# Performance work log

Hardware: AMD Instinct MI355X
Metric: run time of the kernel (lower is better)

Reference implementation:

```python
import jax, jax.numpy as jnp
import numpy as np

B, L, D_MODEL, H = 2, 2048, 1024, 16
HD = D_MODEL // H  # head dim = 64


def setup_inputs() -> dict:
    key = jax.random.key(0)
    ks = jax.random.split(key, 11)
    s = 1.0 / np.sqrt(D_MODEL)
    inp = {
        "Q": jax.random.normal(ks[0], (B, L, D_MODEL), jnp.float32),
        "K": jax.random.normal(ks[1], (B, L, D_MODEL), jnp.float32),
        "V": jax.random.normal(ks[2], (B, L, D_MODEL), jnp.float32),
        "Wq": jax.random.normal(ks[3], (D_MODEL, D_MODEL), jnp.float32) * s,
        "bq": jnp.zeros((D_MODEL,), jnp.float32),
        "Wk": jax.random.normal(ks[4], (D_MODEL, D_MODEL), jnp.float32) * s,
        "bk": jnp.zeros((D_MODEL,), jnp.float32),
        "Wv": jax.random.normal(ks[5], (D_MODEL, D_MODEL), jnp.float32) * s,
        "bv": jnp.zeros((D_MODEL,), jnp.float32),
        "Wo": jax.random.normal(ks[6], (D_MODEL, D_MODEL), jnp.float32) * s,
        "bo": jnp.zeros((D_MODEL,), jnp.float32),
    }
    return inp


def _split_heads(x):
    # [B, L, H*D] -> [B, H, L, D]
    return x.reshape(B, L, H, HD).transpose(0, 2, 1, 3)


def reference(Q, K, V, Wq, bq, Wk, bk, Wv, bv, Wo, bo):
    q = _split_heads(Q @ Wq.T + bq)
    k = _split_heads(K @ Wk.T + bk)
    v = _split_heads(V @ Wv.T + bv)
    scale = 1.0 / jnp.sqrt(jnp.asarray(HD, q.dtype))
    # full [B, H, L, L] score matrix, as in the original bmm->softmax->bmm
    scores = jnp.einsum("bhqd,bhkd->bhqk", q, k) * scale
    attn = jax.nn.softmax(scores, axis=-1)
    o = jnp.einsum("bhqk,bhkd->bhqd", attn, v)
    o = o.transpose(0, 2, 1, 3).reshape(B, L, D_MODEL)  # concat heads
    return o @ Wo.T + bo
```

## Files before the change

kernel.cpp:

```cpp
#include <hip/hip_runtime.h>
#include <math.h>
#include <stdint.h>

typedef __bf16 bf16_t;
typedef __attribute__((ext_vector_type(2))) __bf16 bf16x2;
typedef __attribute__((ext_vector_type(8))) __bf16 bf16x8;
typedef __attribute__((ext_vector_type(4))) float f32x4;
typedef __attribute__((ext_vector_type(16))) float f32x16;
typedef __attribute__((address_space(1))) unsigned int gu32;
typedef __attribute__((address_space(3))) unsigned int lu32;

#define MFMA16(a, b, c) __builtin_amdgcn_mfma_f32_16x16x32_bf16((a), (b), (c), 0, 0, 0)
#define MFMA32(a, b, c) __builtin_amdgcn_mfma_f32_32x32x16_bf16((a), (b), (c), 0, 0, 0)

__device__ __forceinline__ void gll16(const void* g, void* l) {
    __builtin_amdgcn_global_load_lds((const gu32*)(uintptr_t)g,
                                     (lu32*)(uintptr_t)l, 16, 0, 0);
}

__device__ __forceinline__ bf16x8 ld_frag68(const bf16_t* p) {
    union { bf16x8 v; uint2 u[2]; } r;
    r.u[0] = *(const uint2*)p;
    r.u[1] = *(const uint2*)(p + 4);
    return r.v;
}

__global__ __launch_bounds__(256) void convert_all(
    const float* __restrict__ Q, const float* __restrict__ K, const float* __restrict__ V,
    const float* __restrict__ Wq, const float* __restrict__ Wk, const float* __restrict__ Wv,
    const float* __restrict__ Wo, bf16_t* __restrict__ dst) {
    size_t e0 = (size_t)blockIdx.x * 2048;
    const float* src; size_t off;
    if (e0 < 4194304)       { src = Q;  off = e0; }
    else if (e0 < 8388608)  { src = K;  off = e0 - 4194304; }
    else if (e0 < 12582912) { src = V;  off = e0 - 8388608; }
    else if (e0 < 13631488) { src = Wq; off = e0 - 12582912; }
    else if (e0 < 14680064) { src = Wk; off = e0 - 13631488; }
    else if (e0 < 15728640) { src = Wv; off = e0 - 14680064; }
    else                    { src = Wo; off = e0 - 15728640; }
#pragma unroll
    for (int p = 0; p < 2; ++p) {
        int t = p * 1024 + threadIdx.x * 4;
        float4 v = *(const float4*)(src + off + t);
        union { ushort4 u; bf16_t h[4]; } pk;
        pk.h[0] = (bf16_t)v.x; pk.h[1] = (bf16_t)v.y;
        pk.h[2] = (bf16_t)v.z; pk.h[3] = (bf16_t)v.w;
        *(ushort4*)(dst + e0 + t) = pk.u;
    }
}

__global__ __launch_bounds__(256) void qkv_gemm(
    const bf16_t* __restrict__ Qb, const bf16_t* __restrict__ Kb, const bf16_t* __restrict__ Vb,
    const bf16_t* __restrict__ Wqb, const bf16_t* __restrict__ Wkb, const bf16_t* __restrict__ Wvb,
    const float* __restrict__ bq, const float* __restrict__ bk, const float* __restrict__ bv,
    bf16_t* __restrict__ qo, bf16_t* __restrict__ ko, bf16_t* __restrict__ vT) {
    constexpr int Kdim = 1024, N = 1024;
    __shared__ __attribute__((aligned(16))) bf16_t smem[4 * 128 * 64];

    const int tid = threadIdx.x, wave = tid >> 6, lane = tid & 63;
    const int z = blockIdx.z;
    const bf16_t* A = (z == 0) ? Qb : (z == 1) ? Kb : Vb;
    const bf16_t* W = (z == 0) ? Wqb : (z == 1) ? Wkb : Wvb;
    const float* bias = (z == 0) ? bq : (z == 1) ? bk : bv;
    const int bm = blockIdx.x * 128, bn = blockIdx.y * 128;
    const int l16 = lane & 15, quad = lane >> 4;
    const int wm = (wave >> 1) * 64, wn = (wave & 1) * 64;
    const int grow = lane >> 3;
    const int gcol = (((lane & 7) ^ grow)) * 8;
    const int rsw = l16 & 7;

    f32x4 acc[4][4] = {};

    auto stage = [&](int k0, bf16_t* As, bf16_t* Bs) {
#pragma unroll
        for (int j = 0; j < 4; ++j) {
            int chunk = wave * 4 + j;
            int row = chunk * 8 + grow;
            gll16(A + (size_t)(bm + row) * Kdim + k0 + gcol, As + chunk * 512);
            gll16(W + (size_t)(bn + row) * Kdim + k0 + gcol, Bs + chunk * 512);
        }
    };
    auto compute = [&](const bf16_t* As, const bf16_t* Bs) {
#pragma unroll
        for (int ks = 0; ks < 64; ks += 32) {
            const int so = (((ks >> 3) + quad) ^ rsw) * 8;
            bf16x8 af[4], bf[4];
#pragma unroll
            for (int i = 0; i < 4; ++i)
                af[i] = *(const bf16x8*)&As[(wm + i * 16 + l16) * 64 + so];
#pragma unroll
            for (int i = 0; i < 4; ++i)
                bf[i] = *(const bf16x8*)&Bs[(wn + i * 16 + l16) * 64 + so];
#pragma unroll
            for (int i = 0; i < 4; ++i)
#pragma unroll
                for (int j = 0; j < 4; ++j)
                    acc[i][j] = MFMA16(af[i], bf[j], acc[i][j]);
        }
    };

    stage(0, smem, smem + 8192);
    asm volatile("s_waitcnt vmcnt(0)" ::: "memory");
    __builtin_amdgcn_s_barrier();
    int cur = 0;
    for (int t = 0; t < 15; ++t) {
        bf16_t* nb = smem + (cur ^ 1) * 16384;
        stage((t + 1) * 64, nb, nb + 8192);
        bf16_t* cb = smem + cur * 16384;
        compute(cb, cb + 8192);
        asm volatile("s_waitcnt vmcnt(0)" ::: "memory");
        __builtin_amdgcn_s_barrier();
        cur ^= 1;
    }
    {
        bf16_t* cb = smem + cur * 16384;
        compute(cb, cb + 8192);
    }

    if (z < 2) {
        bf16_t* outp = (z == 0) ? qo : ko;
        const float sc = (z == 0) ? 0.18033688011112042f : 1.0f;
        constexpr int RST = 132;
#pragma unroll
        for (int p = 0; p < 2; ++p) {
            __syncthreads();
            if ((wave >> 1) == p) {
#pragma unroll
                for (int mi = 0; mi < 4; ++mi)
#pragma unroll
                    for (int nj = 0; nj < 4; ++nj) {
                        int col = wn + nj * 16 + l16;
                        float bv_ = bias[bn + col];
#pragma unroll
                        for (int r = 0; r < 4; ++r) {
                            int rp = mi * 16 + quad * 4 + r;
                            smem[rp * RST + col] = (bf16_t)((acc[mi][nj][r] + bv_) * sc);
                        }
                    }
            }
            __syncthreads();
            int rp = tid >> 2;
            int cb2 = (tid & 3) * 32;
            int row = bm + p * 64 + rp;
#pragma unroll
            for (int j = 0; j < 4; ++j) {
                uint2 lo = *(const uint2*)&smem[rp * RST + cb2 + j * 8];
                uint2 hi = *(const uint2*)&smem[rp * RST + cb2 + j * 8 + 4];
                *(uint4*)&outp[(size_t)row * N + bn + cb2 + j * 8] =
                    make_uint4(lo.x, lo.y, hi.x, hi.y);
            }
        }
    } else {
#pragma unroll
        for (int mi = 0; mi < 4; ++mi)
#pragma unroll
            for (int nj = 0; nj < 4; ++nj) {
                int col = bn + wn + nj * 16 + l16;
                int h = col >> 6, d = col & 63;
                float bv_ = bias[col];
                int row0 = bm + wm + mi * 16 + quad * 4;
                int bb = row0 >> 11, l = row0 & 2047;
                int lb = (l & ~12) | ((l & 4) << 1) | ((l & 8) >> 1);
                union { ushort4 u; bf16_t h4[4]; } pk;
#pragma unroll
                for (int r = 0; r < 4; ++r) pk.h4[r] = (bf16_t)(acc[mi][nj][r] + bv_);
                *(ushort4*)&vT[(((size_t)bb * 16 + h) * 64 + d) * 2048 + lb] = pk.u;
            }
    }
}

__global__ __launch_bounds__(256) void out_gemm(const bf16_t* __restrict__ Op,
                                                const float* __restrict__ lpp,
                                                const bf16_t* __restrict__ W,
                                                const float* __restrict__ bias,
                                                float* __restrict__ out) {
    constexpr int Kdim = 1024, N = 1024;
    __shared__ __attribute__((aligned(16))) bf16_t smem[2 * 12288];
    const int tid = threadIdx.x, wave = tid >> 6, lane = tid & 63;
    const int bm = blockIdx.x * 64, bn = blockIdx.y * 128;
    const int l16 = lane & 15, quad = lane >> 4;
    const int wm = (wave >> 1) * 32, wn = (wave & 1) * 64;
    const int grow = lane >> 3;
    const int gcol = (((lane & 7) ^ grow)) * 8;
    const int rsw = l16 & 7;
    f32x4 acc[2][4] = {};

    const int arow0 = bm + (wave * 2 + 0) * 8 + grow;
    const int arow1 = bm + (wave * 2 + 1) * 8 + grow;

    uint4 a0p, a0q, a1p, a1q;
    float ivn0, ivn1;

    auto loadA = [&](int k0) {
        const int h = k0 >> 6;
        a0p = *(const uint4*)(Op + (size_t)arow0 * Kdim + k0 + gcol);
        a0q = *(const uint4*)(Op + 4194304 + (size_t)arow0 * Kdim + k0 + gcol);
        a1p = *(const uint4*)(Op + (size_t)arow1 * Kdim + k0 + gcol);
        a1q = *(const uint4*)(Op + 4194304 + (size_t)arow1 * Kdim + k0 + gcol);
        const int li0 = ((arow0 >> 11) * 16 + h) * 2048 + (arow0 & 2047);
        const int li1 = ((arow1 >> 11) * 16 + h) * 2048 + (arow1 & 2047);
        ivn0 = 1.f / (lpp[li0] + lpp[65536 + li0]);
        ivn1 = 1.f / (lpp[li1] + lpp[65536 + li1]);
    };
    auto writeA = [&](bf16_t* As) {
        union { uint4 u; bf16_t h8[8]; } x, y, w0, w1;
        x.u = a0p; y.u = a0q;
#pragma unroll
        for (int i = 0; i < 8; ++i)
            w0.h8[i] = (bf16_t)(((float)x.h8[i] + (float)y.h8[i]) * ivn0);
        x.u = a1p; y.u = a1q;
#pragma unroll
        for (int i = 0; i < 8; ++i)
            w1.h8[i] = (bf16_t)(((float)x.h8[i] + (float)y.h8[i]) * ivn1);
        *(uint4*)&As[(wave * 2 + 0) * 512 + lane * 8] = w0.u;
        *(uint4*)&As[(wave * 2 + 1) * 512 + lane * 8] = w1.u;
    };
    auto stageW = [&](int k0, bf16_t* Bs) {
#pragma unroll
        for (int j = 0; j < 4; ++j) {
            int chunk = wave * 4 + j;
            int row = chunk * 8 + grow;
            gll16(W + (size_t)(bn + row) * Kdim + k0 + gcol, Bs + chunk * 512);
        }
    };
    auto compute = [&](const bf16_t* As, const bf16_t* Bs) {
#pragma unroll
        for (int ks = 0; ks < 64; ks += 32) {
            const int so0 = (((ks >> 3) + quad) ^ rsw) * 8;
            bf16x8 af[2], bf[4];
#pragma unroll
            for (int i = 0; i < 2; ++i)
                af[i] = *(const bf16x8*)&As[(wm + i * 16 + l16) * 64 + so0];
#pragma unroll
            for (int i = 0; i < 4; ++i)
                bf[i] = *(const bf16x8*)&Bs[(wn + i * 16 + l16) * 64 + so0];
#pragma unroll
            for (int i = 0; i < 2; ++i)
#pragma unroll
                for (int j = 0; j < 4; ++j)
                    acc[i][j] = MFMA16(af[i], bf[j], acc[i][j]);
        }
    };

    loadA(0);
    stageW(0, smem + 4096);
    writeA(smem);
    __syncthreads();
    int cur = 0;
    for (int t = 0; t < 15; ++t) {
        bf16_t* nb = smem + (cur ^ 1) * 12288;
        loadA((t + 1) * 64);
        stageW((t + 1) * 64, nb + 4096);
        bf16_t* cb = smem + cur * 12288;
        compute(cb, cb + 4096);
        writeA(nb);
        asm volatile("s_waitcnt vmcnt(0)" ::: "memory");
        __syncthreads();
        cur ^= 1;
    }
    {
        bf16_t* cb = smem + cur * 12288;
        compute(cb, cb + 4096);
    }

#pragma unroll
    for (int mi = 0; mi < 2; ++mi)
#pragma unroll
        for (int nj = 0; nj < 4; ++nj) {
            int col = bn + wn + nj * 16 + l16;
            float bv_ = bias[col];
#pragma unroll
            for (int r = 0; r < 4; ++r) {
                int row = bm + wm + mi * 16 + quad * 4 + r;
                out[(size_t)row * N + col] = acc[mi][nj][r] + bv_;
            }
        }
}

__global__ __launch_bounds__(256, 2) void attn8(const bf16_t* __restrict__ qo,
                                                const bf16_t* __restrict__ ko,
                                                const bf16_t* __restrict__ vT,
                                                bf16_t* __restrict__ Op,
                                                float* __restrict__ lpp) {
    constexpr int L = 2048, D = 1024, ST = 68;
    constexpr int BUF = 2 * 64 * ST;
    __shared__ __attribute__((aligned(16))) bf16_t smem[2 * BUF];

    const int tid = threadIdx.x, wave = tid >> 6, lane = tid & 63;
    const int l31 = lane & 31, hi = lane >> 5;
    const int b = blockIdx.x >> 4, h = blockIdx.x & 15;
    const int q0 = blockIdx.y * 256;
    const int split = blockIdx.z;
    bf16_t* Opart = Op + (size_t)split * 4194304;
    float* lpart = lpp + split * 65536;

    const int rloc = tid >> 2, cg = tid & 3;
    const bf16_t* kbase = ko + ((size_t)b * L + rloc) * D + h * 64 + cg * 16;
    const bf16_t* vbase = vT + (((size_t)b * 16 + h) * 64 + rloc) * L + cg * 16;

    bf16x8 qfa[4], qfb[4];
    {
        const bf16_t* qa = qo + ((size_t)b * L + q0 + wave * 32 + l31) * D + h * 64 + hi * 8;
        const bf16_t* qb2 = qa + (size_t)128 * D;
#pragma unroll
        for (int ks = 0; ks < 4; ++ks) {
            qfa[ks] = *(const bf16x8*)(qa + ks * 16);
            qfb[ks] = *(const bf16x8*)(qb2 + ks * 16);
        }
    }

    f32x16 o0a{}, o1a{}, o0b{}, o1b{};
    float lpla = 0.f, lplb = 0.f;

    const int kt0 = split * 16, kt1 = kt0 + 16;

    uint4 ka, kc, va, vc;
    auto gload = [&](int kt) {
        const size_t koff = (size_t)(kt * 64) * D;
        const int voff = kt * 64;
        ka = *(const uint4*)(kbase + koff);
        kc = *(const uint4*)(kbase + koff + 8);
        va = *(const uint4*)(vbase + voff);
        vc = *(const uint4*)(vbase + voff + 8);
    };
    auto swrite = [&](bf16_t* buf) {
        bf16_t* kd = &buf[rloc * ST + cg * 16];
        bf16_t* vd = &buf[64 * ST + rloc * ST + cg * 16];
        *(uint2*)(kd + 0)  = make_uint2(ka.x, ka.y);
        *(uint2*)(kd + 4)  = make_uint2(ka.z, ka.w);
        *(uint2*)(kd + 8)  = make_uint2(kc.x, kc.y);
        *(uint2*)(kd + 12) = make_uint2(kc.z, kc.w);
        *(uint2*)(vd + 0)  = make_uint2(va.x, va.y);
        *(uint2*)(vd + 4)  = make_uint2(va.z, va.w);
        *(uint2*)(vd + 8)  = make_uint2(vc.x, vc.y);
        *(uint2*)(vd + 12) = make_uint2(vc.z, vc.w);
    };

    gload(kt0);
    swrite(smem);
    gload(kt0 + 1 < kt1 ? kt0 + 1 : kt1 - 1);
    asm volatile("s_waitcnt lgkmcnt(0)" ::: "memory");
    __builtin_amdgcn_s_barrier();

    int cur = 0;
    for (int kt = kt0; kt < kt1; ++kt) {
        swrite(smem + (cur ^ 1) * BUF);
        gload(kt + 2 < kt1 ? kt + 2 : kt1 - 1);
        const bf16_t* ksm = smem + cur * BUF;
        const bf16_t* vsm = ksm + 64 * ST;

        f32x16 s0a{}, s1a{}, s0b{}, s1b{};
        __builtin_amdgcn_s_setprio(1);
#pragma unroll
        for (int ks = 0; ks < 4; ++ks) {
            bf16x8 k0 = ld_frag68(&ksm[l31 * ST + ks * 16 + hi * 8]);
            bf16x8 k1 = ld_frag68(&ksm[(32 + l31) * ST + ks * 16 + hi * 8]);
            s0a = MFMA32(k0, qfa[ks], s0a);
            s1a = MFMA32(k1, qfa[ks], s1a);
            s0b = MFMA32(k0, qfb[ks], s0b);
            s1b = MFMA32(k1, qfb[ks], s1b);
        }
        __builtin_amdgcn_s_setprio(0);

#pragma unroll
        for (int t = 0; t < 4; ++t) {
            union { bf16x8 v; bf16_t e[8]; } pfa, pfb;
#pragma unroll
            for (int j = 0; j < 8; ++j) {
                float sva = (t < 2) ? s0a[(t & 1) * 8 + j] : s1a[(t & 1) * 8 + j];
                float svb = (t < 2) ? s0b[(t & 1) * 8 + j] : s1b[(t & 1) * 8 + j];
                float pa = __builtin_amdgcn_exp2f(sva);
                float pb = __builtin_amdgcn_exp2f(svb);
                lpla += pa; lplb += pb;
                pfa.e[j] = (bf16_t)pa;
                pfb.e[j] = (bf16_t)pb;
            }
            bf16x8 v0 = ld_frag68(&vsm[l31 * ST + t * 16 + hi * 8]);
            bf16x8 v1 = ld_frag68(&vsm[(32 + l31) * ST + t * 16 + hi * 8]);
            __builtin_amdgcn_s_setprio(1);
            o0a = MFMA32(v0, pfa.v, o0a);
            o1a = MFMA32(v1, pfa.v, o1a);
            o0b = MFMA32(v0, pfb.v, o0b);
            o1b = MFMA32(v1, pfb.v, o1b);
            __builtin_amdgcn_s_setprio(0);
        }

        asm volatile("s_waitcnt lgkmcnt(0)" ::: "memory");
        __builtin_amdgcn_s_barrier();
        cur ^= 1;
    }

    lpla += __shfl_xor(lpla, 32, 64);
    lplb += __shfl_xor(lplb, 32, 64);
    if (hi == 0) {
        lpart[((size_t)b * 16 + h) * 2048 + q0 + wave * 32 + l31] = lpla;
        lpart[((size_t)b * 16 + h) * 2048 + q0 + 128 + wave * 32 + l31] = lplb;
    }

    __syncthreads();
    bf16_t* ew = smem + wave * (32 * ST);
#pragma unroll
    for (int r = 0; r < 16; r += 2) {
        int d = (r & 3) + 8 * (r >> 2) + 4 * hi;
        *(bf16x2*)&ew[l31 * ST + d] = bf16x2{(bf16_t)o0a[r], (bf16_t)o0a[r + 1]};
        *(bf16x2*)&ew[l31 * ST + 32 + d] = bf16x2{(bf16_t)o1a[r], (bf16_t)o1a[r + 1]};
    }
#pragma unroll
    for (int p = 0; p < 4; ++p) {
        int rr = p * 8 + (lane >> 3);
        int cc = (lane & 7) * 8;
        uint2 lo = *(const uint2*)&ew[rr * ST + cc];
        uint2 hi2 = *(const uint2*)&ew[rr * ST + cc + 4];
        *(uint4*)&Opart[((size_t)b * L + q0 + wave * 32 + rr) * D + h * 64 + cc] =
            make_uint4(lo.x, lo.y, hi2.x, hi2.y);
    }
#pragma unroll
    for (int r = 0; r < 16; r += 2) {
        int d = (r & 3) + 8 * (r >> 2) + 4 * hi;
        *(bf16x2*)&ew[l31 * ST + d] = bf16x2{(bf16_t)o0b[r], (bf16_t)o0b[r + 1]};
        *(bf16x2*)&ew[l31 * ST + 32 + d] = bf16x2{(bf16_t)o1b[r], (bf16_t)o1b[r + 1]};
    }
#pragma unroll
    for (int p = 0; p < 4; ++p) {
        int rr = p * 8 + (lane >> 3);
        int cc = (lane & 7) * 8;
        uint2 lo = *(const uint2*)&ew[rr * ST + cc];
        uint2 hi2 = *(const uint2*)&ew[rr * ST + cc + 4];
        *(uint4*)&Opart[((size_t)b * L + q0 + 128 + wave * 32 + rr) * D + h * 64 + cc] =
            make_uint4(lo.x, lo.y, hi2.x, hi2.y);
    }
}

extern "C" void kernel_launch(void* const* d_in, const int* in_sizes, int n_in,
                              void* d_out, int out_size, void* d_ws, size_t ws_size,
                              hipStream_t stream) {
    const float* Q  = (const float*)d_in[0];
    const float* Kx = (const float*)d_in[1];
    const float* V  = (const float*)d_in[2];
    const float* Wq = (const float*)d_in[3];
    const float* bq = (const float*)d_in[4];
    const float* Wk = (const float*)d_in[5];
    const float* bk = (const float*)d_in[6];
    const float* Wv = (const float*)d_in[7];
    const float* bv = (const float*)d_in[8];
    const float* Wo = (const float*)d_in[9];
    const float* bo = (const float*)d_in[10];

    bf16_t* ws0 = (bf16_t*)d_ws;
    bf16_t* Qb  = ws0;
    bf16_t* Kb  = ws0 + 4194304;
    bf16_t* Vb  = ws0 + 8388608;
    bf16_t* Wqb = ws0 + 12582912;
    bf16_t* Wkb = ws0 + 13631488;
    bf16_t* Wvb = ws0 + 14680064;
    bf16_t* Wob = ws0 + 15728640;
    bf16_t* vT  = ws0 + 16777216;
    bf16_t* Op  = Qb;
    float*  lpp = (float*)Wqb;
    bf16_t* qo = (bf16_t*)d_out;
    bf16_t* ko = qo + 4194304;

    convert_all<<<8192, 256, 0, stream>>>(Q, Kx, V, Wq, Wk, Wv, Wo, ws0);
    qkv_gemm<<<dim3(32, 8, 3), 256, 0, stream>>>(Qb, Kb, Vb, Wqb, Wkb, Wvb,
                                                 bq, bk, bv, qo, ko, vT);
    attn8<<<dim3(32, 8, 2), 256, 0, stream>>>(qo, ko, vT, Op, lpp);
    out_gemm<<<dim3(64, 8), 256, 0, stream>>>(Op, lpp, Wob, bo, (float*)d_out);
}
```

Baseline: 221.1 us.

## Enlarge QKV GEMM tiles to 256x256 with 8 waves and interleaved prefetch

The QKV projection GEMM moves from 128x128 tiles with 4 waves to 256x256 tiles with 8 waves. Each wave now computes a 128x64 sub-tile. The main loop is restructured so the A and B prefetch loads are split and interleaved between MFMA groups, and s_setprio is raised around the MFMA bursts. The aim is more reuse per loaded byte and better overlap of loads with compute. The cost is 128KB of LDS, higher register pressure from the doubled accumulators, and only 192 blocks, which may not fill all CUs.

```diff
diff --git a/kernel.cpp b/kernel.cpp
--- a/kernel.cpp
+++ b/kernel.cpp
@@ -49,84 +49,137 @@
     }
 }
 
-__global__ __launch_bounds__(256) void qkv_gemm(
+__global__ __launch_bounds__(512, 2) void qkv_gemm(
     const bf16_t* __restrict__ Qb, const bf16_t* __restrict__ Kb, const bf16_t* __restrict__ Vb,
     const bf16_t* __restrict__ Wqb, const bf16_t* __restrict__ Wkb, const bf16_t* __restrict__ Wvb,
     const float* __restrict__ bq, const float* __restrict__ bk, const float* __restrict__ bv,
     bf16_t* __restrict__ qo, bf16_t* __restrict__ ko, bf16_t* __restrict__ vT) {
     constexpr int Kdim = 1024, N = 1024;
-    __shared__ __attribute__((aligned(16))) bf16_t smem[4 * 128 * 64];
+    __shared__ __attribute__((aligned(16))) bf16_t smem[2 * 32768];
 
     const int tid = threadIdx.x, wave = tid >> 6, lane = tid & 63;
     const int z = blockIdx.z;
     const bf16_t* A = (z == 0) ? Qb : (z == 1) ? Kb : Vb;
     const bf16_t* W = (z == 0) ? Wqb : (z == 1) ? Wkb : Wvb;
     const float* bias = (z == 0) ? bq : (z == 1) ? bk : bv;
-    const int bm = blockIdx.x * 128, bn = blockIdx.y * 128;
+    const int bm = blockIdx.x * 256, bn = blockIdx.y * 256;
     const int l16 = lane & 15, quad = lane >> 4;
-    const int wm = (wave >> 1) * 64, wn = (wave & 1) * 64;
+    const int wr = wave >> 2, wc = wave & 3;
+    const int wm = wr * 128, wn = wc * 64;
     const int grow = lane >> 3;
     const int gcol = (((lane & 7) ^ grow)) * 8;
     const int rsw = l16 & 7;
 
-    f32x4 acc[4][4] = {};
-
-    auto stage = [&](int k0, bf16_t* As, bf16_t* Bs) {
+    f32x4 acc[8][4] = {};
+
+    auto stageA = [&](int k0, bf16_t* As) {
 #pragma unroll
         for (int j = 0; j < 4; ++j) {
             int chunk = wave * 4 + j;
             int row = chunk * 8 + grow;
             gll16(A + (size_t)(bm + row) * Kdim + k0 + gcol, As + chunk * 512);
+        }
+    };
+    auto stageB = [&](int k0, bf16_t* Bs) {
+#pragma unroll
+        for (int j = 0; j < 4; ++j) {
+            int chunk = wave * 4 + j;
+            int row = chunk * 8 + grow;
             gll16(W + (size_t)(bn + row) * Kdim + k0 + gcol, Bs + chunk * 512);
         }
     };
-    auto compute = [&](const bf16_t* As, const bf16_t* Bs) {
-#pragma unroll
-        for (int ks = 0; ks < 64; ks += 32) {
-            const int so = (((ks >> 3) + quad) ^ rsw) * 8;
-            bf16x8 af[4], bf[4];
-#pragma unroll
-            for (int i = 0; i < 4; ++i)
-                af[i] = *(const bf16x8*)&As[(wm + i * 16 + l16) * 64 + so];
-#pragma unroll
-            for (int i = 0; i < 4; ++i)
-                bf[i] = *(const bf16x8*)&Bs[(wn + i * 16 + l16) * 64 + so];
+
+    stageA(0, smem);
+    stageB(0, smem + 16384);
+    asm volatile("s_waitcnt vmcnt(0)" ::: "memory");
+    __builtin_amdgcn_s_barrier();
+
+    int cur = 0;
+    for (int t = 0; t < 16; ++t) {
+        const bf16_t* cA = smem + cur * 32768;
+        const bf16_t* cB = cA + 16384;
+        bf16_t* nA = smem + (cur ^ 1) * 32768;
+        bf16_t* nB = nA + 16384;
+        const int k1 = (t + 1) * 64;
+        const bool pf = (t < 15);
+
+        bf16x8 af[4], bf[4];
+        if (pf) stageA(k1, nA);
+        {
+            const int so = ((0 + quad) ^ rsw) * 8;
+#pragma unroll
+            for (int i = 0; i < 4; ++i)
+                bf[i] = *(const bf16x8*)&cB[(wn + i * 16 + l16) * 64 + so];
+#pragma unroll
+            for (int i = 0; i < 4; ++i)
+                af[i] = *(const bf16x8*)&cA[(wm + i * 16 + l16) * 64 + so];
+            __builtin_amdgcn_s_setprio(1);
 #pragma unroll
             for (int i = 0; i < 4; ++i)
 #pragma unroll
                 for (int j = 0; j < 4; ++j)
                     acc[i][j] = MFMA16(af[i], bf[j], acc[i][j]);
-        }
-    };
-
-    stage(0, smem, smem + 8192);
-    asm volatile("s_waitcnt vmcnt(0)" ::: "memory");
-    __builtin_amdgcn_s_barrier();
-    int cur = 0;
-    for (int t = 0; t < 15; ++t) {
-        bf16_t* nb = smem + (cur ^ 1) * 16384;
-        stage((t + 1) * 64, nb, nb + 8192);
-        bf16_t* cb = smem + cur * 16384;
-        compute(cb, cb + 8192);
+            __builtin_amdgcn_s_setprio(0);
+        }
+        if (pf) stageB(k1, nB);
+        {
+            const int so = ((0 + quad) ^ rsw) * 8;
+#pragma unroll
+            for (int i = 0; i < 4; ++i)
+                af[i] = *(const bf16x8*)&cA[(wm + 64 + i * 16 + l16) * 64 + so];
+            __builtin_amdgcn_s_setprio(1);
+#pragma unroll
+            for (int i = 0; i < 4; ++i)
+#pragma unroll
+                for (int j = 0; j < 4; ++j)
+                    acc[4 + i][j] = MFMA16(af[i], bf[j], acc[4 + i][j]);
+            __builtin_amdgcn_s_setprio(0);
+        }
+        {
+            const int so = ((4 + quad) ^ rsw) * 8;
+#pragma unroll
+            for (int i = 0; i < 4; ++i)
+                bf[i] = *(const bf16x8*)&cB[(wn + i * 16 + l16) * 64 + so];
+#pragma unroll
+            for (int i = 0; i < 4; ++i)
+                af[i] = *(const bf16x8*)&cA[(wm + i * 16 + l16) * 64 + so];
+            __builtin_amdgcn_s_setprio(1);
+#pragma unroll
+            for (int i = 0; i < 4; ++i)
+#pragma unroll
+                for (int j = 0; j < 4; ++j)
+                    acc[i][j] = MFMA16(af[i], bf[j], acc[i][j]);
+            __builtin_amdgcn_s_setprio(0);
+        }
+        {
+            const int so = ((4 + quad) ^ rsw) * 8;
+#pragma unroll
+            for (int i = 0; i < 4; ++i)
+                af[i] = *(const bf16x8*)&cA[(wm + 64 + i * 16 + l16) * 64 + so];
+            __builtin_amdgcn_s_setprio(1);
+#pragma unroll
+            for (int i = 0; i < 4; ++i)
+#pragma unroll
+                for (int j = 0; j < 4; ++j)
+                    acc[4 + i][j] = MFMA16(af[i], bf[j], acc[4 + i][j]);
+            __builtin_amdgcn_s_setprio(0);
+        }
+
         asm volatile("s_waitcnt vmcnt(0)" ::: "memory");
         __builtin_amdgcn_s_barrier();
         cur ^= 1;
     }
-    {
-        bf16_t* cb = smem + cur * 16384;
-        compute(cb, cb + 8192);
-    }
 
     if (z < 2) {
         bf16_t* outp = (z == 0) ? qo : ko;
         const float sc = (z == 0) ? 0.18033688011112042f : 1.0f;
-        constexpr int RST = 132;
+        constexpr int RST = 264;
 #pragma unroll
         for (int p = 0; p < 2; ++p) {
             __syncthreads();
-            if ((wave >> 1) == p) {
-#pragma unroll
-                for (int mi = 0; mi < 4; ++mi)
+            if (wr == p) {
+#pragma unroll
+                for (int mi = 0; mi < 8; ++mi)
 #pragma unroll
                     for (int nj = 0; nj < 4; ++nj) {
                         int col = wn + nj * 16 + l16;
@@ -140,10 +193,10 @@
             }
             __syncthreads();
             int rp = tid >> 2;
-            int cb2 = (tid & 3) * 32;
-            int row = bm + p * 64 + rp;
-#pragma unroll
-            for (int j = 0; j < 4; ++j) {
+            int cb2 = (tid & 3) * 64;
+            int row = bm + p * 128 + rp;
+#pragma unroll
+            for (int j = 0; j < 8; ++j) {
                 uint2 lo = *(const uint2*)&smem[rp * RST + cb2 + j * 8];
                 uint2 hi = *(const uint2*)&smem[rp * RST + cb2 + j * 8 + 4];
                 *(uint4*)&outp[(size_t)row * N + bn + cb2 + j * 8] =
@@ -152,7 +205,7 @@
         }
     } else {
 #pragma unroll
-        for (int mi = 0; mi < 4; ++mi)
+        for (int mi = 0; mi < 8; ++mi)
 #pragma unroll
             for (int nj = 0; nj < 4; ++nj) {
                 int col = bn + wn + nj * 16 + l16;
@@ -461,7 +514,7 @@
     bf16_t* ko = qo + 4194304;
 
     convert_all<<<8192, 256, 0, stream>>>(Q, Kx, V, Wq, Wk, Wv, Wo, ws0);
-    qkv_gemm<<<dim3(32, 8, 3), 256, 0, stream>>>(Qb, Kb, Vb, Wqb, Wkb, Wvb,
+    qkv_gemm<<<dim3(16, 4, 3), 512, 0, stream>>>(Qb, Kb, Vb, Wqb, Wkb, Wvb,
                                                  bq, bk, bv, qo, ko, vT);
     attn8<<<dim3(32, 8, 2), 256, 0, stream>>>(qo, ko, vT, Op, lpp);
     out_gemm<<<dim3(64, 8), 256, 0, stream>>>(Op, lpp, Wob, bo, (float*)d_out);
```

After: 212.9 us. -3.7%, faster.

## Fuse fp32-to-bf16 conversion into GEMM tile loads, drop convert kernel

Applied to the files above, without the earlier changes.

Removes the separate convert_all kernel and has qkv_gemm and out_gemm read fp32 inputs and weights directly. The tiles are converted to bf16 in registers and written to LDS, replacing the global_load_lds async copies. This saves one launch and a full write-then-reread of bf16 copies of Q/K/V and the weights. In exchange each GEMM reads twice the bytes per tile, repeated across the N-tile blocks, uses more registers for staging, and does conversion ALU work inside the main loop.

```diff
diff --git a/kernel.cpp b/kernel.cpp
--- a/kernel.cpp
+++ b/kernel.cpp
@@ -7,16 +7,9 @@
 typedef __attribute__((ext_vector_type(8))) __bf16 bf16x8;
 typedef __attribute__((ext_vector_type(4))) float f32x4;
 typedef __attribute__((ext_vector_type(16))) float f32x16;
-typedef __attribute__((address_space(1))) unsigned int gu32;
-typedef __attribute__((address_space(3))) unsigned int lu32;
 
 #define MFMA16(a, b, c) __builtin_amdgcn_mfma_f32_16x16x32_bf16((a), (b), (c), 0, 0, 0)
 #define MFMA32(a, b, c) __builtin_amdgcn_mfma_f32_32x32x16_bf16((a), (b), (c), 0, 0, 0)
-
-__device__ __forceinline__ void gll16(const void* g, void* l) {
-    __builtin_amdgcn_global_load_lds((const gu32*)(uintptr_t)g,
-                                     (lu32*)(uintptr_t)l, 16, 0, 0);
-}
 
 __device__ __forceinline__ bf16x8 ld_frag68(const bf16_t* p) {
     union { bf16x8 v; uint2 u[2]; } r;
@@ -25,33 +18,18 @@
     return r.v;
 }
 
-__global__ __launch_bounds__(256) void convert_all(
+__device__ __forceinline__ uint4 pack8(float4 x, float4 y) {
+    union { uint4 u; bf16_t h[8]; } r;
+    r.h[0] = (bf16_t)x.x; r.h[1] = (bf16_t)x.y;
+    r.h[2] = (bf16_t)x.z; r.h[3] = (bf16_t)x.w;
+    r.h[4] = (bf16_t)y.x; r.h[5] = (bf16_t)y.y;
+    r.h[6] = (bf16_t)y.z; r.h[7] = (bf16_t)y.w;
+    return r.u;
+}
+
+__global__ __launch_bounds__(256) void qkv_gemm(
     const float* __restrict__ Q, const float* __restrict__ K, const float* __restrict__ V,
     const float* __restrict__ Wq, const float* __restrict__ Wk, const float* __restrict__ Wv,
-    const float* __restrict__ Wo, bf16_t* __restrict__ dst) {
-    size_t e0 = (size_t)blockIdx.x * 2048;
-    const float* src; size_t off;
-    if (e0 < 4194304)       { src = Q;  off = e0; }
-    else if (e0 < 8388608)  { src = K;  off = e0 - 4194304; }
-    else if (e0 < 12582912) { src = V;  off = e0 - 8388608; }
-    else if (e0 < 13631488) { src = Wq; off = e0 - 12582912; }
-    else if (e0 < 14680064) { src = Wk; off = e0 - 13631488; }
-    else if (e0 < 15728640) { src = Wv; off = e0 - 14680064; }
-    else                    { src = Wo; off = e0 - 15728640; }
-#pragma unroll
-    for (int p = 0; p < 2; ++p) {
-        int t = p * 1024 + threadIdx.x * 4;
-        float4 v = *(const float4*)(src + off + t);
-        union { ushort4 u; bf16_t h[4]; } pk;
-        pk.h[0] = (bf16_t)v.x; pk.h[1] = (bf16_t)v.y;
-        pk.h[2] = (bf16_t)v.z; pk.h[3] = (bf16_t)v.w;
-        *(ushort4*)(dst + e0 + t) = pk.u;
-    }
-}
-
-__global__ __launch_bounds__(256) void qkv_gemm(
-    const bf16_t* __restrict__ Qb, const bf16_t* __restrict__ Kb, const bf16_t* __restrict__ Vb,
-    const bf16_t* __restrict__ Wqb, const bf16_t* __restrict__ Wkb, const bf16_t* __restrict__ Wvb,
     const float* __restrict__ bq, const float* __restrict__ bk, const float* __restrict__ bv,
     bf16_t* __restrict__ qo, bf16_t* __restrict__ ko, bf16_t* __restrict__ vT) {
     constexpr int Kdim = 1024, N = 1024;
@@ -59,8 +37,8 @@
 
     const int tid = threadIdx.x, wave = tid >> 6, lane = tid & 63;
     const int z = blockIdx.z;
-    const bf16_t* A = (z == 0) ? Qb : (z == 1) ? Kb : Vb;
-    const bf16_t* W = (z == 0) ? Wqb : (z == 1) ? Wkb : Wvb;
+    const float* Af = (z == 0) ? Q : (z == 1) ? K : V;
+    const float* Wf = (z == 0) ? Wq : (z == 1) ? Wk : Wv;
     const float* bias = (z == 0) ? bq : (z == 1) ? bk : bv;
     const int bm = blockIdx.x * 128, bn = blockIdx.y * 128;
     const int l16 = lane & 15, quad = lane >> 4;
@@ -70,14 +48,25 @@
     const int rsw = l16 & 7;
 
     f32x4 acc[4][4] = {};
-
-    auto stage = [&](int k0, bf16_t* As, bf16_t* Bs) {
+    float4 sa[8], sw[8];
+
+    auto loadT = [&](int k0) {
 #pragma unroll
         for (int j = 0; j < 4; ++j) {
-            int chunk = wave * 4 + j;
-            int row = chunk * 8 + grow;
-            gll16(A + (size_t)(bm + row) * Kdim + k0 + gcol, As + chunk * 512);
-            gll16(W + (size_t)(bn + row) * Kdim + k0 + gcol, Bs + chunk * 512);
+            int row = (wave * 4 + j) * 8 + grow;
+            const float* pa = Af + (size_t)(bm + row) * Kdim + k0 + gcol;
+            const float* pw = Wf + (size_t)(bn + row) * Kdim + k0 + gcol;
+            sa[2 * j]     = *(const float4*)pa;
+            sa[2 * j + 1] = *(const float4*)(pa + 4);
+            sw[2 * j]     = *(const float4*)pw;
+            sw[2 * j + 1] = *(const float4*)(pw + 4);
+        }
+    };
+    auto writeT = [&](bf16_t* As, bf16_t* Bs) {
+#pragma unroll
+        for (int j = 0; j < 4; ++j) {
+            *(uint4*)&As[(wave * 4 + j) * 512 + lane * 8] = pack8(sa[2 * j], sa[2 * j + 1]);
+            *(uint4*)&Bs[(wave * 4 + j) * 512 + lane * 8] = pack8(sw[2 * j], sw[2 * j + 1]);
         }
     };
     auto compute = [&](const bf16_t* As, const bf16_t* Bs) {
@@ -99,17 +88,17 @@
         }
     };
 
-    stage(0, smem, smem + 8192);
-    asm volatile("s_waitcnt vmcnt(0)" ::: "memory");
-    __builtin_amdgcn_s_barrier();
+    loadT(0);
+    writeT(smem, smem + 8192);
+    __syncthreads();
     int cur = 0;
     for (int t = 0; t < 15; ++t) {
-        bf16_t* nb = smem + (cur ^ 1) * 16384;
-        stage((t + 1) * 64, nb, nb + 8192);
+        loadT((t + 1) * 64);
         bf16_t* cb = smem + cur * 16384;
         compute(cb, cb + 8192);
-        asm volatile("s_waitcnt vmcnt(0)" ::: "memory");
-        __builtin_amdgcn_s_barrier();
+        bf16_t* nb = smem + (cur ^ 1) * 16384;
+        writeT(nb, nb + 8192);
+        __syncthreads();
         cur ^= 1;
     }
     {
@@ -171,7 +160,7 @@
 
 __global__ __launch_bounds__(256) void out_gemm(const bf16_t* __restrict__ Op,
                                                 const float* __restrict__ lpp,
-                                                const bf16_t* __restrict__ W,
+                                                const float* __restrict__ Wf,
                                                 const float* __restrict__ bias,
                                                 float* __restrict__ out) {
     constexpr int Kdim = 1024, N = 1024;
@@ -190,6 +179,7 @@
 
     uint4 a0p, a0q, a1p, a1q;
     float ivn0, ivn1;
+    float4 swv[8];
 
     auto loadA = [&](int k0) {
         const int h = k0 >> 6;
@@ -202,6 +192,15 @@
         ivn0 = 1.f / (lpp[li0] + lpp[65536 + li0]);
         ivn1 = 1.f / (lpp[li1] + lpp[65536 + li1]);
     };
+    auto loadW = [&](int k0) {
+#pragma unroll
+        for (int j = 0; j < 4; ++j) {
+            int row = bn + (wave * 4 + j) * 8 + grow;
+            const float* pw = Wf + (size_t)row * Kdim + k0 + gcol;
+            swv[2 * j]     = *(const float4*)pw;
+            swv[2 * j + 1] = *(const float4*)(pw + 4);
+        }
+    };
     auto writeA = [&](bf16_t* As) {
         union { uint4 u; bf16_t h8[8]; } x, y, w0, w1;
         x.u = a0p; y.u = a0q;
@@ -215,13 +214,10 @@
         *(uint4*)&As[(wave * 2 + 0) * 512 + lane * 8] = w0.u;
         *(uint4*)&As[(wave * 2 + 1) * 512 + lane * 8] = w1.u;
     };
-    auto stageW = [&](int k0, bf16_t* Bs) {
-#pragma unroll
-        for (int j = 0; j < 4; ++j) {
-            int chunk = wave * 4 + j;
-            int row = chunk * 8 + grow;
-            gll16(W + (size_t)(bn + row) * Kdim + k0 + gcol, Bs + chunk * 512);
-        }
+    auto writeW = [&](bf16_t* Bs) {
+#pragma unroll
+        for (int j = 0; j < 4; ++j)
+            *(uint4*)&Bs[(wave * 4 + j) * 512 + lane * 8] = pack8(swv[2 * j], swv[2 * j + 1]);
     };
     auto compute = [&](const bf16_t* As, const bf16_t* Bs) {
 #pragma unroll
@@ -243,18 +239,19 @@
     };
 
     loadA(0);
-    stageW(0, smem + 4096);
+    loadW(0);
     writeA(smem);
+    writeW(smem + 4096);
     __syncthreads();
     int cur = 0;
     for (int t = 0; t < 15; ++t) {
-        bf16_t* nb = smem + (cur ^ 1) * 12288;
         loadA((t + 1) * 64);
-        stageW((t + 1) * 64, nb + 4096);
+        loadW((t + 1) * 64);
         bf16_t* cb = smem + cur * 12288;
         compute(cb, cb + 4096);
+        bf16_t* nb = smem + (cur ^ 1) * 12288;
         writeA(nb);
-        asm volatile("s_waitcnt vmcnt(0)" ::: "memory");
+        writeW(nb + 4096);
         __syncthreads();
         cur ^= 1;
     }
@@ -447,22 +444,14 @@
     const float* bo = (const float*)d_in[10];
 
     bf16_t* ws0 = (bf16_t*)d_ws;
-    bf16_t* Qb  = ws0;
-    bf16_t* Kb  = ws0 + 4194304;
-    bf16_t* Vb  = ws0 + 8388608;
-    bf16_t* Wqb = ws0 + 12582912;
-    bf16_t* Wkb = ws0 + 13631488;
-    bf16_t* Wvb = ws0 + 14680064;
-    bf16_t* Wob = ws0 + 15728640;
-    bf16_t* vT  = ws0 + 16777216;
-    bf16_t* Op  = Qb;
-    float*  lpp = (float*)Wqb;
+    bf16_t* Op  = ws0;
+    float*  lpp = (float*)(ws0 + 8388608);
+    bf16_t* vT  = ws0 + 8388608 + 262144;
     bf16_t* qo = (bf16_t*)d_out;
     bf16_t* ko = qo + 4194304;
 
-    convert_all<<<8192, 256, 0, stream>>>(Q, Kx, V, Wq, Wk, Wv, Wo, ws0);
-    qkv_gemm<<<dim3(32, 8, 3), 256, 0, stream>>>(Qb, Kb, Vb, Wqb, Wkb, Wvb,
+    qkv_gemm<<<dim3(32, 8, 3), 256, 0, stream>>>(Q, Kx, V, Wq, Wk, Wv,
                                                  bq, bk, bv, qo, ko, vT);
     attn8<<<dim3(32, 8, 2), 256, 0, stream>>>(qo, ko, vT, Op, lpp);
-    out_gemm<<<dim3(64, 8), 256, 0, stream>>>(Op, lpp, Wob, bo, (float*)d_out);
-}
+    out_gemm<<<dim3(64, 8), 256, 0, stream>>>(Op, lpp, Wo, bo, (float*)d_out);
+}
```

Result: slower. 257.7 us (+16.6%).
